# Kernel tuning notes

Hardware: AMD Instinct MI355X
Metric: run time of the kernel (lower is better)

Reference implementation:

```python
import jax, jax.numpy as jnp
import numpy as np

EMBED = 64
HEADS = 4
HEAD_DIM = EMBED // HEADS
N, T = 1024, 36


def setup_inputs() -> dict:
    key = jax.random.key(0)
    ks = jax.random.split(key, 8)
    scale = 1.0 / np.sqrt(HEAD_DIM)
    return {
        "values": jax.random.normal(ks[0], (N, T, EMBED), dtype=jnp.float32),
        "keys": jax.random.normal(ks[1], (N, T, EMBED), dtype=jnp.float32),
        "query": jax.random.normal(ks[2], (N, T, EMBED), dtype=jnp.float32),
        "Wv": jax.random.normal(ks[3], (HEAD_DIM, HEAD_DIM), dtype=jnp.float32) * scale,
        "Wk": jax.random.normal(ks[4], (HEAD_DIM, HEAD_DIM), dtype=jnp.float32) * scale,
        "Wq": jax.random.normal(ks[5], (HEAD_DIM, HEAD_DIM), dtype=jnp.float32) * scale,
        "Wo": jax.random.normal(ks[6], (EMBED, EMBED), dtype=jnp.float32) * (1.0 / np.sqrt(EMBED)),
        "bo": jax.random.normal(ks[7], (EMBED,), dtype=jnp.float32) * 0.01,
    }


def reference(values, keys, query, Wv, Wk, Wq, Wo, bo):
    n, t, c = query.shape
    h, d = HEADS, HEAD_DIM
    v = values.reshape(n, t, h, d)
    k = keys.reshape(n, t, h, d)
    q = query.reshape(n, t, h, d)
    # nn.Linear(head_dim, head_dim, bias=False): x @ W.T
    v = jnp.einsum('nthd,ed->nthe', v, Wv)
    k = jnp.einsum('nthd,ed->nthe', k, Wk)
    q = jnp.einsum('nthd,ed->nthe', q, Wq)
    # attention over the node dim: energy [N_q, N_k, T, H]
    energy = jnp.einsum('qthd,kthd->qkth', q, k)
    attention = jax.nn.softmax(energy / jnp.sqrt(jnp.float32(c)), axis=1)
    out = jnp.einsum('qkth,kthd->qthd', attention, v).reshape(n, t, h * d)
    return out @ Wo.T + bo
```

## Files before the change

kernel.cpp:

```cpp
#include <hip/hip_runtime.h>
#include <math.h>

#define N_NODES 1024
#define T_STEPS 36
#define KTILE   128
#define KSTR2   24
#define VTSTR   136
#define WOS     72
#define OBS2    72
#define YSTR    67

typedef __bf16  bf16x8 __attribute__((ext_vector_type(8)));
typedef float   f32x4  __attribute__((ext_vector_type(4)));

#define MFMA_BF16 __builtin_amdgcn_mfma_f32_16x16x32_bf16
#define PERM_HI 0x07060302u
#define PERM_LO 0x05040100u

__device__ __forceinline__ unsigned short bf16_rne(float f) {
    unsigned int u = __float_as_uint(f);
    u += 0x7FFFu + ((u >> 16) & 1u);
    return (unsigned short)(u >> 16);
}
__device__ __forceinline__ float bf16_tof(unsigned short h) {
    return __uint_as_float(((unsigned int)h) << 16);
}
__device__ __forceinline__ unsigned int split_pack(float a) {
    unsigned short hi = bf16_rne(a);
    unsigned short lo = bf16_rne(a - bf16_tof(hi));
    return ((unsigned int)hi << 16) | lo;
}

__global__ __launch_bounds__(128) void proj5_kernel(
    const float* __restrict__ vin, const float* __restrict__ kin, const float* __restrict__ qin,
    const float* __restrict__ Wv, const float* __restrict__ Wk, const float* __restrict__ Wq,
    unsigned short* __restrict__ qhi, unsigned short* __restrict__ qlo,
    unsigned short* __restrict__ khi, unsigned short* __restrict__ klo,
    unsigned short* __restrict__ vthi, unsigned short* __restrict__ vtlo)
{
    __shared__ float sW[256];
    __shared__ unsigned int ys[128 * YSTR];

    const int tid = threadIdx.x;
    const int mat = blockIdx.y;
    const int nt  = blockIdx.x & 15;
    const int tt  = blockIdx.x >> 4;
    const int n0  = nt * 64, t0 = tt * 2;

    const float* in = (mat == 0) ? vin : (mat == 1) ? kin : qin;
    const float* W  = (mat == 0) ? Wv  : (mat == 1) ? Wk  : Wq;
    sW[tid] = W[tid]; sW[tid + 128] = W[tid + 128];
    __syncthreads();

    {
        const int nl = tid >> 1, tl = tid & 1;
        const size_t p = ((size_t)(n0 + nl)) * T_STEPS + (t0 + tl);
        const float4* src = (const float4*)(in + p * 64);
        float x[64];
        #pragma unroll
        for (int i = 0; i < 16; ++i) {
            float4 f = src[i];
            x[4*i] = f.x; x[4*i+1] = f.y; x[4*i+2] = f.z; x[4*i+3] = f.w;
        }
        const float scale = (mat == 2) ? 0.18033688011112042f : 1.0f;
        unsigned int* yrow = &ys[tid * YSTR];
        #pragma unroll
        for (int e = 0; e < 16; ++e) {
            float4 w0 = *(const float4*)&sW[e*16+0],  w1 = *(const float4*)&sW[e*16+4];
            float4 w2 = *(const float4*)&sW[e*16+8],  w3 = *(const float4*)&sW[e*16+12];
            #pragma unroll
            for (int hd = 0; hd < 4; ++hd) {
                const float* xr = &x[hd*16];
                float a = xr[0]*w0.x;
                a = fmaf(xr[1],w0.y,a);  a = fmaf(xr[2],w0.z,a);  a = fmaf(xr[3],w0.w,a);
                a = fmaf(xr[4],w1.x,a);  a = fmaf(xr[5],w1.y,a);  a = fmaf(xr[6],w1.z,a);  a = fmaf(xr[7],w1.w,a);
                a = fmaf(xr[8],w2.x,a);  a = fmaf(xr[9],w2.y,a);  a = fmaf(xr[10],w2.z,a); a = fmaf(xr[11],w2.w,a);
                a = fmaf(xr[12],w3.x,a); a = fmaf(xr[13],w3.y,a); a = fmaf(xr[14],w3.z,a); a = fmaf(xr[15],w3.w,a);
                yrow[hd*16 + e] = split_pack(a * scale);
            }
        }
    }
    __syncthreads();

    if (mat != 0) {
        unsigned short* ohi = (mat == 1) ? khi : qhi;
        unsigned short* olo = (mat == 1) ? klo : qlo;
        const int nl2 = tid >> 1, eh = tid & 1;
        #pragma unroll
        for (int pass = 0; pass < 8; ++pass) {
            const int tl2 = pass & 1, hd = pass >> 1;
            const unsigned int* yr = &ys[(nl2*2 + tl2) * YSTR + hd*16 + eh*8];
            unsigned int u0 = yr[0], u1 = yr[1], u2 = yr[2], u3 = yr[3];
            unsigned int u4 = yr[4], u5 = yr[5], u6 = yr[6], u7 = yr[7];
            uint4 hi4, lo4;
            hi4.x = __builtin_amdgcn_perm(u1, u0, PERM_HI);
            hi4.y = __builtin_amdgcn_perm(u3, u2, PERM_HI);
            hi4.z = __builtin_amdgcn_perm(u5, u4, PERM_HI);
            hi4.w = __builtin_amdgcn_perm(u7, u6, PERM_HI);
            lo4.x = __builtin_amdgcn_perm(u1, u0, PERM_LO);
            lo4.y = __builtin_amdgcn_perm(u3, u2, PERM_LO);
            lo4.z = __builtin_amdgcn_perm(u5, u4, PERM_LO);
            lo4.w = __builtin_amdgcn_perm(u7, u6, PERM_LO);
            const int th = (t0 + tl2) * 4 + hd;
            const size_t off = ((size_t)th * N_NODES + n0 + nl2) * 16 + eh * 8;
            *(uint4*)(ohi + off) = hi4;
            *(uint4*)(olo + off) = lo4;
        }
    } else {
        const int e = tid >> 3, ng = tid & 7;
        #pragma unroll
        for (int pass = 0; pass < 8; ++pass) {
            const int tl2 = pass & 1, hd = pass >> 1;
            unsigned int u[8];
            #pragma unroll
            for (int j = 0; j < 8; ++j)
                u[j] = ys[((ng*8 + j)*2 + tl2) * YSTR + hd*16 + e];
            uint4 hi4, lo4;
            hi4.x = __builtin_amdgcn_perm(u[1], u[0], PERM_HI);
            hi4.y = __builtin_amdgcn_perm(u[3], u[2], PERM_HI);
            hi4.z = __builtin_amdgcn_perm(u[5], u[4], PERM_HI);
            hi4.w = __builtin_amdgcn_perm(u[7], u[6], PERM_HI);
            lo4.x = __builtin_amdgcn_perm(u[1], u[0], PERM_LO);
            lo4.y = __builtin_amdgcn_perm(u[3], u[2], PERM_LO);
            lo4.z = __builtin_amdgcn_perm(u[5], u[4], PERM_LO);
            lo4.w = __builtin_amdgcn_perm(u[7], u[6], PERM_LO);
            const int th = (t0 + tl2) * 4 + hd;
            const size_t off = ((size_t)th * 16 + e) * N_NODES + n0 + ng * 8;
            *(uint4*)(vthi + off) = hi4;
            *(uint4*)(vtlo + off) = lo4;
        }
    }
}

__global__ __launch_bounds__(128, 4) void attn_mfma4_kernel(
    const unsigned short* __restrict__ qhi, const unsigned short* __restrict__ qlo,
    const unsigned short* __restrict__ khi, const unsigned short* __restrict__ klo,
    const unsigned short* __restrict__ vthi, const unsigned short* __restrict__ vtlo,
    unsigned short* __restrict__ obh, unsigned short* __restrict__ obl)
{
    __shared__ unsigned short khi_s[KTILE * KSTR2];
    __shared__ unsigned short klo_s[KTILE * KSTR2];
    __shared__ unsigned short vthi_s[16 * VTSTR];
    __shared__ unsigned short vtlo_s[16 * VTSTR];

    const int tid  = threadIdx.x;
    const int wave = tid >> 6, lane = tid & 63;
    const int m = lane & 15, quad = lane >> 4;

    const int bid = blockIdx.x;
    const int th  = bid % 144;
    const int qb  = bid / 144;
    const int t   = th >> 2, hd = th & 3;
    const int q0  = qb * 64;
    const size_t base_th = (size_t)th * N_NODES;

    const bf16x8 bzero = {};
    bf16x8 b1q[2], b2q[2];
    #pragma unroll
    for (int g = 0; g < 2; ++g) {
        const int qrow = q0 + wave * 32 + g * 16 + m;
        b1q[g] = *(const bf16x8*)(qhi + (base_th + qrow) * 16 + (quad & 1) * 8);
        b2q[g] = (quad < 2)
            ? *(const bf16x8*)(qlo + (base_th + qrow) * 16 + (quad & 1) * 8) : bzero;
    }

    union { unsigned short su[8]; bf16x8 v; } onesu;
    #pragma unroll
    for (int i = 0; i < 8; ++i) onesu.su[i] = 0x3F80;
    const bf16x8 bones = onesu.v;

    f32x4 og[2]   = {{0.f,0.f,0.f,0.f},{0.f,0.f,0.f,0.f}};
    f32x4 lacc[2] = {{0.f,0.f,0.f,0.f},{0.f,0.f,0.f,0.f}};
    const unsigned short* kbase = (quad < 2) ? khi_s : klo_s;
    const int koff = m * KSTR2 + (quad & 1) * 8;
    const int voff = m * VTSTR + quad * 8;

    const int vsel = tid >> 6, vd = (tid >> 2) & 15, vpart = tid & 3;
    const unsigned short* vsrc0 = (vsel ? vtlo : vthi)
        + ((size_t)th * 16 + vd) * N_NODES + vpart * 32;
    unsigned short* vdst = (vsel ? vtlo_s : vthi_s) + vd * VTSTR + vpart * 32;

    for (int kt = 0; kt < N_NODES; kt += KTILE) {
        __syncthreads();
        {
            const uint4* gh = (const uint4*)(khi + (base_th + kt + tid) * 16);
            const uint4* gl = (const uint4*)(klo + (base_th + kt + tid) * 16);
            uint4 a0 = gh[0], a1 = gh[1], c0 = gl[0], c1 = gl[1];
            *(uint4*)&khi_s[tid * KSTR2]     = a0;
            *(uint4*)&khi_s[tid * KSTR2 + 8] = a1;
            *(uint4*)&klo_s[tid * KSTR2]     = c0;
            *(uint4*)&klo_s[tid * KSTR2 + 8] = c1;
        }
        {
            const unsigned short* src = vsrc0 + kt;
            uint4 a0 = ((const uint4*)src)[0], a1 = ((const uint4*)src)[1];
            uint4 a2 = ((const uint4*)src)[2], a3 = ((const uint4*)src)[3];
            *(uint2*)&vdst[0]  = make_uint2(a0.x, a0.y);
            *(uint2*)&vdst[8]  = make_uint2(a0.z, a0.w);
            *(uint2*)&vdst[16] = make_uint2(a1.x, a1.y);
            *(uint2*)&vdst[24] = make_uint2(a1.z, a1.w);
            *(uint2*)&vdst[4]  = make_uint2(a2.x, a2.y);
            *(uint2*)&vdst[12] = make_uint2(a2.z, a2.w);
            *(uint2*)&vdst[20] = make_uint2(a3.x, a3.y);
            *(uint2*)&vdst[28] = make_uint2(a3.z, a3.w);
        }
        __syncthreads();

        #pragma unroll
        for (int c = 0; c < 4; ++c) {
            bf16x8 a0 = *(const bf16x8*)(kbase + (2*c    ) * 16 * KSTR2 + koff);
            bf16x8 a1 = *(const bf16x8*)(kbase + (2*c + 1) * 16 * KSTR2 + koff);
            bf16x8 vh = *(const bf16x8*)&vthi_s[voff + c * 32];
            bf16x8 vl = *(const bf16x8*)&vtlo_s[voff + c * 32];
            #pragma unroll
            for (int g = 0; g < 2; ++g) {
                f32x4 s0 = MFMA_BF16(a0, b1q[g], (f32x4){0.f,0.f,0.f,0.f}, 0, 0, 0);
                s0 = MFMA_BF16(a0, b2q[g], s0, 0, 0, 0);
                f32x4 s1 = MFMA_BF16(a1, b1q[g], (f32x4){0.f,0.f,0.f,0.f}, 0, 0, 0);
                s1 = MFMA_BF16(a1, b2q[g], s1, 0, 0, 0);
                union { __bf16 b[8]; bf16x8 v; } ap;
                ap.b[0] = (__bf16)__builtin_amdgcn_exp2f(s0[0]);
                ap.b[1] = (__bf16)__builtin_amdgcn_exp2f(s0[1]);
                ap.b[2] = (__bf16)__builtin_amdgcn_exp2f(s0[2]);
                ap.b[3] = (__bf16)__builtin_amdgcn_exp2f(s0[3]);
                ap.b[4] = (__bf16)__builtin_amdgcn_exp2f(s1[0]);
                ap.b[5] = (__bf16)__builtin_amdgcn_exp2f(s1[1]);
                ap.b[6] = (__bf16)__builtin_amdgcn_exp2f(s1[2]);
                ap.b[7] = (__bf16)__builtin_amdgcn_exp2f(s1[3]);
                lacc[g] = MFMA_BF16(ap.v, bones, lacc[g], 0, 0, 0);
                og[g]   = MFMA_BF16(ap.v, vh, og[g], 0, 0, 0);
                og[g]   = MFMA_BF16(ap.v, vl, og[g], 0, 0, 0);
            }
        }
    }

    #pragma unroll
    for (int g = 0; g < 2; ++g) {
        #pragma unroll
        for (int r = 0; r < 4; ++r) {
            const float val = og[g][r] * __builtin_amdgcn_rcpf(lacc[g][r]);
            const int row = q0 + wave * 32 + g * 16 + quad * 4 + r;
            const size_t off = ((size_t)row * T_STEPS + t) * 64 + hd * 16 + m;
            unsigned short hh = bf16_rne(val);
            obh[off] = hh;
            obl[off] = bf16_rne(val - bf16_tof(hh));
        }
    }
}

__global__ __launch_bounds__(256) void outproj_mfma_kernel(
    const unsigned short* __restrict__ obh, const unsigned short* __restrict__ obl,
    const float* __restrict__ Wo, const float* __restrict__ bo,
    float* __restrict__ out)
{
    __shared__ unsigned short woh[64 * WOS], wol[64 * WOS];
    __shared__ unsigned short oth[64 * OBS2], otl[64 * OBS2];
    __shared__ float sb[64];
    const int tid = threadIdx.x;

    #pragma unroll
    for (int i = 0; i < 16; ++i) {
        int idx = tid + 256 * i;
        int r = idx >> 6, c = idx & 63;
        float w = Wo[idx];
        unsigned short hh = bf16_rne(w);
        woh[r * WOS + c] = hh;
        wol[r * WOS + c] = bf16_rne(w - bf16_tof(hh));
    }
    if (tid < 64) sb[tid] = bo[tid];

    const size_t p0 = (size_t)blockIdx.x * 64;
    #pragma unroll
    for (int i = 0; i < 2; ++i) {
        int idx = tid + 256 * i;
        int r = idx >> 3, c = (idx & 7) * 8;
        *(uint4*)&oth[r * OBS2 + c] = *(const uint4*)(obh + (p0 + r) * 64 + c);
        *(uint4*)&otl[r * OBS2 + c] = *(const uint4*)(obl + (p0 + r) * 64 + c);
    }
    __syncthreads();

    const int wave = tid >> 6, lane = tid & 63;
    const int m = lane & 15, quad = lane >> 4;
    const int r0 = wave * 16;

    bf16x8 ah[2], al[2];
    #pragma unroll
    for (int kh = 0; kh < 2; ++kh) {
        ah[kh] = *(const bf16x8*)&oth[(r0 + m) * OBS2 + kh * 32 + quad * 8];
        al[kh] = *(const bf16x8*)&otl[(r0 + m) * OBS2 + kh * 32 + quad * 8];
    }

    f32x4 acc[4] = {{0,0,0,0},{0,0,0,0},{0,0,0,0},{0,0,0,0}};
    #pragma unroll
    for (int jt = 0; jt < 4; ++jt) {
        #pragma unroll
        for (int kh = 0; kh < 2; ++kh) {
            bf16x8 bh = *(const bf16x8*)&woh[(jt * 16 + m) * WOS + kh * 32 + quad * 8];
            bf16x8 bl = *(const bf16x8*)&wol[(jt * 16 + m) * WOS + kh * 32 + quad * 8];
            acc[jt] = MFMA_BF16(ah[kh], bh, acc[jt], 0, 0, 0);
            acc[jt] = MFMA_BF16(al[kh], bh, acc[jt], 0, 0, 0);
            acc[jt] = MFMA_BF16(ah[kh], bl, acc[jt], 0, 0, 0);
        }
    }

    #pragma unroll
    for (int jt = 0; jt < 4; ++jt) {
        const float b = sb[jt * 16 + m];
        #pragma unroll
        for (int r = 0; r < 4; ++r)
            out[(p0 + r0 + quad * 4 + r) * 64 + jt * 16 + m] = acc[jt][r] + b;
    }
}

extern "C" void kernel_launch(void* const* d_in, const int* in_sizes, int n_in,
                              void* d_out, int out_size, void* d_ws, size_t ws_size,
                              hipStream_t stream)
{
    (void)in_sizes; (void)n_in; (void)out_size; (void)ws_size;
    const float* values = (const float*)d_in[0];
    const float* keys   = (const float*)d_in[1];
    const float* query  = (const float*)d_in[2];
    const float* Wv     = (const float*)d_in[3];
    const float* Wk     = (const float*)d_in[4];
    const float* Wq     = (const float*)d_in[5];
    const float* Wo     = (const float*)d_in[6];
    const float* bo     = (const float*)d_in[7];

    const size_t TOT = (size_t)144 * N_NODES * 16;
    unsigned short* ws16 = (unsigned short*)d_ws;
    unsigned short* qhi  = ws16;
    unsigned short* qlo  = ws16 + 1*TOT;
    unsigned short* khi  = ws16 + 2*TOT;
    unsigned short* klo  = ws16 + 3*TOT;
    unsigned short* vthi = ws16 + 4*TOT;
    unsigned short* vtlo = ws16 + 5*TOT;
    unsigned short* obh  = ws16 + 6*TOT;
    unsigned short* obl  = ws16 + 7*TOT;

    proj5_kernel<<<dim3(288, 3), 128, 0, stream>>>(values, keys, query, Wv, Wk, Wq,
                                                   qhi, qlo, khi, klo, vthi, vtlo);
    attn_mfma4_kernel<<<dim3(16 * 144), 128, 0, stream>>>(qhi, qlo, khi, klo, vthi, vtlo,
                                                          obh, obl);
    outproj_mfma_kernel<<<dim3(576), 256, 0, stream>>>(obh, obl, Wo, bo, (float*)d_out);
}
```

Baseline: 138.0 us.

## Read K fragments from global directly, prefetch V tiles, and shrink projection staging

The attention kernel no longer stages K hi/lo tiles through shared memory. Each lane loads its MFMA K fragment straight from global memory, and the V tile for the next iteration is prefetched into registers, which cuts LDS traffic and lets the occupancy hint rise from 4 to 5 blocks. The projection kernel writes Q/K outputs directly from registers and processes V one head at a time through a smaller LDS staging buffer. The trade-off is uncoalesced-ish global fragment loads for K that now rely on cache hits, plus extra barriers in the V projection path.

```diff
diff --git a/kernel.cpp b/kernel.cpp
--- a/kernel.cpp
+++ b/kernel.cpp
@@ -4,11 +4,10 @@
 #define N_NODES 1024
 #define T_STEPS 36
 #define KTILE   128
-#define KSTR2   24
 #define VTSTR   136
 #define WOS     72
 #define OBS2    72
-#define YSTR    67
+#define YSTR6   17
 
 typedef __bf16  bf16x8 __attribute__((ext_vector_type(8)));
 typedef float   f32x4  __attribute__((ext_vector_type(4)));
@@ -25,13 +24,8 @@
 __device__ __forceinline__ float bf16_tof(unsigned short h) {
     return __uint_as_float(((unsigned int)h) << 16);
 }
-__device__ __forceinline__ unsigned int split_pack(float a) {
-    unsigned short hi = bf16_rne(a);
-    unsigned short lo = bf16_rne(a - bf16_tof(hi));
-    return ((unsigned int)hi << 16) | lo;
-}
-
-__global__ __launch_bounds__(128) void proj5_kernel(
+
+__global__ __launch_bounds__(128) void proj6_kernel(
     const float* __restrict__ vin, const float* __restrict__ kin, const float* __restrict__ qin,
     const float* __restrict__ Wv, const float* __restrict__ Wk, const float* __restrict__ Wq,
     unsigned short* __restrict__ qhi, unsigned short* __restrict__ qlo,
@@ -39,7 +33,7 @@
     unsigned short* __restrict__ vthi, unsigned short* __restrict__ vtlo)
 {
     __shared__ float sW[256];
-    __shared__ unsigned int ys[128 * YSTR];
+    __shared__ unsigned int ys[128 * YSTR6];
 
     const int tid = threadIdx.x;
     const int mat = blockIdx.y;
@@ -52,94 +46,103 @@
     sW[tid] = W[tid]; sW[tid + 128] = W[tid + 128];
     __syncthreads();
 
-    {
-        const int nl = tid >> 1, tl = tid & 1;
-        const size_t p = ((size_t)(n0 + nl)) * T_STEPS + (t0 + tl);
-        const float4* src = (const float4*)(in + p * 64);
-        float x[64];
-        #pragma unroll
-        for (int i = 0; i < 16; ++i) {
-            float4 f = src[i];
-            x[4*i] = f.x; x[4*i+1] = f.y; x[4*i+2] = f.z; x[4*i+3] = f.w;
-        }
-        const float scale = (mat == 2) ? 0.18033688011112042f : 1.0f;
-        unsigned int* yrow = &ys[tid * YSTR];
-        #pragma unroll
-        for (int e = 0; e < 16; ++e) {
-            float4 w0 = *(const float4*)&sW[e*16+0],  w1 = *(const float4*)&sW[e*16+4];
-            float4 w2 = *(const float4*)&sW[e*16+8],  w3 = *(const float4*)&sW[e*16+12];
+    const int nl = tid >> 1, tl = tid & 1;
+    const int n = n0 + nl, tcur = t0 + tl;
+    const size_t ib = ((size_t)n * T_STEPS + tcur) * 64;
+    const float scale = (mat == 2) ? 0.18033688011112042f : 1.0f;
+
+    if (mat != 0) {
+        unsigned short* ohi = (mat == 1) ? khi : qhi;
+        unsigned short* olo = (mat == 1) ? klo : qlo;
+        #pragma unroll
+        for (int hd = 0; hd < 4; ++hd) {
+            float xr[16];
             #pragma unroll
-            for (int hd = 0; hd < 4; ++hd) {
-                const float* xr = &x[hd*16];
+            for (int i = 0; i < 4; ++i) {
+                float4 f = *(const float4*)(in + ib + hd*16 + 4*i);
+                xr[4*i] = f.x; xr[4*i+1] = f.y; xr[4*i+2] = f.z; xr[4*i+3] = f.w;
+            }
+            union { unsigned short u[16]; uint4 v[2]; } hb, lb;
+            #pragma unroll
+            for (int e = 0; e < 16; ++e) {
+                float4 w0 = *(const float4*)&sW[e*16+0],  w1 = *(const float4*)&sW[e*16+4];
+                float4 w2 = *(const float4*)&sW[e*16+8],  w3 = *(const float4*)&sW[e*16+12];
                 float a = xr[0]*w0.x;
                 a = fmaf(xr[1],w0.y,a);  a = fmaf(xr[2],w0.z,a);  a = fmaf(xr[3],w0.w,a);
                 a = fmaf(xr[4],w1.x,a);  a = fmaf(xr[5],w1.y,a);  a = fmaf(xr[6],w1.z,a);  a = fmaf(xr[7],w1.w,a);
                 a = fmaf(xr[8],w2.x,a);  a = fmaf(xr[9],w2.y,a);  a = fmaf(xr[10],w2.z,a); a = fmaf(xr[11],w2.w,a);
                 a = fmaf(xr[12],w3.x,a); a = fmaf(xr[13],w3.y,a); a = fmaf(xr[14],w3.z,a); a = fmaf(xr[15],w3.w,a);
-                yrow[hd*16 + e] = split_pack(a * scale);
-            }
-        }
-    }
-    __syncthreads();
-
-    if (mat != 0) {
-        unsigned short* ohi = (mat == 1) ? khi : qhi;
-        unsigned short* olo = (mat == 1) ? klo : qlo;
-        const int nl2 = tid >> 1, eh = tid & 1;
-        #pragma unroll
-        for (int pass = 0; pass < 8; ++pass) {
-            const int tl2 = pass & 1, hd = pass >> 1;
-            const unsigned int* yr = &ys[(nl2*2 + tl2) * YSTR + hd*16 + eh*8];
-            unsigned int u0 = yr[0], u1 = yr[1], u2 = yr[2], u3 = yr[3];
-            unsigned int u4 = yr[4], u5 = yr[5], u6 = yr[6], u7 = yr[7];
-            uint4 hi4, lo4;
-            hi4.x = __builtin_amdgcn_perm(u1, u0, PERM_HI);
-            hi4.y = __builtin_amdgcn_perm(u3, u2, PERM_HI);
-            hi4.z = __builtin_amdgcn_perm(u5, u4, PERM_HI);
-            hi4.w = __builtin_amdgcn_perm(u7, u6, PERM_HI);
-            lo4.x = __builtin_amdgcn_perm(u1, u0, PERM_LO);
-            lo4.y = __builtin_amdgcn_perm(u3, u2, PERM_LO);
-            lo4.z = __builtin_amdgcn_perm(u5, u4, PERM_LO);
-            lo4.w = __builtin_amdgcn_perm(u7, u6, PERM_LO);
-            const int th = (t0 + tl2) * 4 + hd;
-            const size_t off = ((size_t)th * N_NODES + n0 + nl2) * 16 + eh * 8;
-            *(uint4*)(ohi + off) = hi4;
-            *(uint4*)(olo + off) = lo4;
+                a *= scale;
+                unsigned short hh = bf16_rne(a);
+                hb.u[e] = hh; lb.u[e] = bf16_rne(a - bf16_tof(hh));
+            }
+            const int th = tcur * 4 + hd;
+            const size_t off = ((size_t)th * N_NODES + n) * 16;
+            *(uint4*)(ohi + off)     = hb.v[0];
+            *(uint4*)(ohi + off + 8) = hb.v[1];
+            *(uint4*)(olo + off)     = lb.v[0];
+            *(uint4*)(olo + off + 8) = lb.v[1];
         }
     } else {
-        const int e = tid >> 3, ng = tid & 7;
-        #pragma unroll
-        for (int pass = 0; pass < 8; ++pass) {
-            const int tl2 = pass & 1, hd = pass >> 1;
-            unsigned int u[8];
-            #pragma unroll
-            for (int j = 0; j < 8; ++j)
-                u[j] = ys[((ng*8 + j)*2 + tl2) * YSTR + hd*16 + e];
-            uint4 hi4, lo4;
-            hi4.x = __builtin_amdgcn_perm(u[1], u[0], PERM_HI);
-            hi4.y = __builtin_amdgcn_perm(u[3], u[2], PERM_HI);
-            hi4.z = __builtin_amdgcn_perm(u[5], u[4], PERM_HI);
-            hi4.w = __builtin_amdgcn_perm(u[7], u[6], PERM_HI);
-            lo4.x = __builtin_amdgcn_perm(u[1], u[0], PERM_LO);
-            lo4.y = __builtin_amdgcn_perm(u[3], u[2], PERM_LO);
-            lo4.z = __builtin_amdgcn_perm(u[5], u[4], PERM_LO);
-            lo4.w = __builtin_amdgcn_perm(u[7], u[6], PERM_LO);
-            const int th = (t0 + tl2) * 4 + hd;
-            const size_t off = ((size_t)th * 16 + e) * N_NODES + n0 + ng * 8;
-            *(uint4*)(vthi + off) = hi4;
-            *(uint4*)(vtlo + off) = lo4;
-        }
-    }
-}
-
-__global__ __launch_bounds__(128, 4) void attn_mfma4_kernel(
+        #pragma unroll
+        for (int hd = 0; hd < 4; ++hd) {
+            {
+                float xr[16];
+                #pragma unroll
+                for (int i = 0; i < 4; ++i) {
+                    float4 f = *(const float4*)(in + ib + hd*16 + 4*i);
+                    xr[4*i] = f.x; xr[4*i+1] = f.y; xr[4*i+2] = f.z; xr[4*i+3] = f.w;
+                }
+                unsigned int* yrow = &ys[tid * YSTR6];
+                #pragma unroll
+                for (int e = 0; e < 16; ++e) {
+                    float4 w0 = *(const float4*)&sW[e*16+0],  w1 = *(const float4*)&sW[e*16+4];
+                    float4 w2 = *(const float4*)&sW[e*16+8],  w3 = *(const float4*)&sW[e*16+12];
+                    float a = xr[0]*w0.x;
+                    a = fmaf(xr[1],w0.y,a);  a = fmaf(xr[2],w0.z,a);  a = fmaf(xr[3],w0.w,a);
+                    a = fmaf(xr[4],w1.x,a);  a = fmaf(xr[5],w1.y,a);  a = fmaf(xr[6],w1.z,a);  a = fmaf(xr[7],w1.w,a);
+                    a = fmaf(xr[8],w2.x,a);  a = fmaf(xr[9],w2.y,a);  a = fmaf(xr[10],w2.z,a); a = fmaf(xr[11],w2.w,a);
+                    a = fmaf(xr[12],w3.x,a); a = fmaf(xr[13],w3.y,a); a = fmaf(xr[14],w3.z,a); a = fmaf(xr[15],w3.w,a);
+                    unsigned short hh = bf16_rne(a);
+                    unsigned short ll = bf16_rne(a - bf16_tof(hh));
+                    yrow[e] = ((unsigned int)hh << 16) | ll;
+                }
+            }
+            __syncthreads();
+            {
+                const int e = tid >> 3, ng = tid & 7;
+                #pragma unroll
+                for (int tl2 = 0; tl2 < 2; ++tl2) {
+                    unsigned int u[8];
+                    #pragma unroll
+                    for (int j = 0; j < 8; ++j)
+                        u[j] = ys[((ng*8 + j)*2 + tl2) * YSTR6 + e];
+                    uint4 hi4, lo4;
+                    hi4.x = __builtin_amdgcn_perm(u[1], u[0], PERM_HI);
+                    hi4.y = __builtin_amdgcn_perm(u[3], u[2], PERM_HI);
+                    hi4.z = __builtin_amdgcn_perm(u[5], u[4], PERM_HI);
+                    hi4.w = __builtin_amdgcn_perm(u[7], u[6], PERM_HI);
+                    lo4.x = __builtin_amdgcn_perm(u[1], u[0], PERM_LO);
+                    lo4.y = __builtin_amdgcn_perm(u[3], u[2], PERM_LO);
+                    lo4.z = __builtin_amdgcn_perm(u[5], u[4], PERM_LO);
+                    lo4.w = __builtin_amdgcn_perm(u[7], u[6], PERM_LO);
+                    const int th = (t0 + tl2) * 4 + hd;
+                    const size_t off = ((size_t)th * 16 + e) * N_NODES + n0 + ng * 8;
+                    *(uint4*)(vthi + off) = hi4;
+                    *(uint4*)(vtlo + off) = lo4;
+                }
+            }
+            if (hd < 3) __syncthreads();
+        }
+    }
+}
+
+__global__ __launch_bounds__(128, 5) void attn_mfma5_kernel(
     const unsigned short* __restrict__ qhi, const unsigned short* __restrict__ qlo,
     const unsigned short* __restrict__ khi, const unsigned short* __restrict__ klo,
     const unsigned short* __restrict__ vthi, const unsigned short* __restrict__ vtlo,
     unsigned short* __restrict__ obh, unsigned short* __restrict__ obl)
 {
-    __shared__ unsigned short khi_s[KTILE * KSTR2];
-    __shared__ unsigned short klo_s[KTILE * KSTR2];
     __shared__ unsigned short vthi_s[16 * VTSTR];
     __shared__ unsigned short vtlo_s[16 * VTSTR];
 
@@ -171,47 +174,40 @@
 
     f32x4 og[2]   = {{0.f,0.f,0.f,0.f},{0.f,0.f,0.f,0.f}};
     f32x4 lacc[2] = {{0.f,0.f,0.f,0.f},{0.f,0.f,0.f,0.f}};
-    const unsigned short* kbase = (quad < 2) ? khi_s : klo_s;
-    const int koff = m * KSTR2 + (quad & 1) * 8;
-    const int voff = m * VTSTR + quad * 8;
-
-    const int vsel = tid >> 6, vd = (tid >> 2) & 15, vpart = tid & 3;
-    const unsigned short* vsrc0 = (vsel ? vtlo : vthi)
+
+    const unsigned short* kfrag = ((quad < 2) ? khi : klo)
+        + (base_th + m) * 16 + (quad & 1) * 8;
+
+    const int vd = (tid >> 2) & 15, vpart = tid & 3;
+    const unsigned short* vsrc0 = (wave ? vtlo : vthi)
         + ((size_t)th * 16 + vd) * N_NODES + vpart * 32;
-    unsigned short* vdst = (vsel ? vtlo_s : vthi_s) + vd * VTSTR + vpart * 32;
+    unsigned short* vdst = (wave ? vtlo_s : vthi_s) + vd * VTSTR + vpart * 32;
+
+    uint4 pf0, pf1, pf2, pf3;
+    { const uint4* s = (const uint4*)vsrc0; pf0 = s[0]; pf1 = s[1]; pf2 = s[2]; pf3 = s[3]; }
 
     for (int kt = 0; kt < N_NODES; kt += KTILE) {
         __syncthreads();
-        {
-            const uint4* gh = (const uint4*)(khi + (base_th + kt + tid) * 16);
-            const uint4* gl = (const uint4*)(klo + (base_th + kt + tid) * 16);
-            uint4 a0 = gh[0], a1 = gh[1], c0 = gl[0], c1 = gl[1];
-            *(uint4*)&khi_s[tid * KSTR2]     = a0;
-            *(uint4*)&khi_s[tid * KSTR2 + 8] = a1;
-            *(uint4*)&klo_s[tid * KSTR2]     = c0;
-            *(uint4*)&klo_s[tid * KSTR2 + 8] = c1;
-        }
-        {
-            const unsigned short* src = vsrc0 + kt;
-            uint4 a0 = ((const uint4*)src)[0], a1 = ((const uint4*)src)[1];
-            uint4 a2 = ((const uint4*)src)[2], a3 = ((const uint4*)src)[3];
-            *(uint2*)&vdst[0]  = make_uint2(a0.x, a0.y);
-            *(uint2*)&vdst[8]  = make_uint2(a0.z, a0.w);
-            *(uint2*)&vdst[16] = make_uint2(a1.x, a1.y);
-            *(uint2*)&vdst[24] = make_uint2(a1.z, a1.w);
-            *(uint2*)&vdst[4]  = make_uint2(a2.x, a2.y);
-            *(uint2*)&vdst[12] = make_uint2(a2.z, a2.w);
-            *(uint2*)&vdst[20] = make_uint2(a3.x, a3.y);
-            *(uint2*)&vdst[28] = make_uint2(a3.z, a3.w);
-        }
+        *(uint2*)&vdst[0]  = make_uint2(pf0.x, pf0.y);
+        *(uint2*)&vdst[8]  = make_uint2(pf0.z, pf0.w);
+        *(uint2*)&vdst[16] = make_uint2(pf1.x, pf1.y);
+        *(uint2*)&vdst[24] = make_uint2(pf1.z, pf1.w);
+        *(uint2*)&vdst[4]  = make_uint2(pf2.x, pf2.y);
+        *(uint2*)&vdst[12] = make_uint2(pf2.z, pf2.w);
+        *(uint2*)&vdst[20] = make_uint2(pf3.x, pf3.y);
+        *(uint2*)&vdst[28] = make_uint2(pf3.z, pf3.w);
         __syncthreads();
+        if (kt + KTILE < N_NODES) {
+            const uint4* s = (const uint4*)(vsrc0 + kt + KTILE);
+            pf0 = s[0]; pf1 = s[1]; pf2 = s[2]; pf3 = s[3];
+        }
 
         #pragma unroll
         for (int c = 0; c < 4; ++c) {
-            bf16x8 a0 = *(const bf16x8*)(kbase + (2*c    ) * 16 * KSTR2 + koff);
-            bf16x8 a1 = *(const bf16x8*)(kbase + (2*c + 1) * 16 * KSTR2 + koff);
-            bf16x8 vh = *(const bf16x8*)&vthi_s[voff + c * 32];
-            bf16x8 vl = *(const bf16x8*)&vtlo_s[voff + c * 32];
+            bf16x8 a0 = *(const bf16x8*)(kfrag + (size_t)(kt + (2*c    )*16) * 16);
+            bf16x8 a1 = *(const bf16x8*)(kfrag + (size_t)(kt + (2*c + 1)*16) * 16);
+            bf16x8 vh = *(const bf16x8*)&vthi_s[m * VTSTR + quad * 8 + c * 32];
+            bf16x8 vl = *(const bf16x8*)&vtlo_s[m * VTSTR + quad * 8 + c * 32];
             #pragma unroll
             for (int g = 0; g < 2; ++g) {
                 f32x4 s0 = MFMA_BF16(a0, b1q[g], (f32x4){0.f,0.f,0.f,0.f}, 0, 0, 0);
@@ -337,9 +333,9 @@
     unsigned short* obh  = ws16 + 6*TOT;
     unsigned short* obl  = ws16 + 7*TOT;
 
-    proj5_kernel<<<dim3(288, 3), 128, 0, stream>>>(values, keys, query, Wv, Wk, Wq,
+    proj6_kernel<<<dim3(288, 3), 128, 0, stream>>>(values, keys, query, Wv, Wk, Wq,
                                                    qhi, qlo, khi, klo, vthi, vtlo);
-    attn_mfma4_kernel<<<dim3(16 * 144), 128, 0, stream>>>(qhi, qlo, khi, klo, vthi, vtlo,
+    attn_mfma5_kernel<<<dim3(16 * 144), 128, 0, stream>>>(qhi, qlo, khi, klo, vthi, vtlo,
                                                           obh, obl);
     outproj_mfma_kernel<<<dim3(576), 256, 0, stream>>>(obh, obl, Wo, bo, (float*)d_out);
 }
```

Result: no change. 138.7 us (+0.6%).

## Load K fragments directly from global and register-prefetch V tiles

Applied to the files above, without the earlier changes.

The attention kernel no longer stages K hi/lo tiles in shared memory. Each lane now reads its MFMA K fragment straight from global memory. The V tile for the next iteration is prefetched into registers right after the barrier, so its global load overlaps the current tile's MFMA work. The launch-bounds occupancy hint rises from 4 to 5 blocks per CU. This cuts LDS traffic and footprint and hides V load latency, at the cost of K reads that may be less coalesced and more register pressure.

```diff
diff --git a/kernel.cpp b/kernel.cpp
--- a/kernel.cpp
+++ b/kernel.cpp
@@ -4,7 +4,6 @@
 #define N_NODES 1024
 #define T_STEPS 36
 #define KTILE   128
-#define KSTR2   24
 #define VTSTR   136
 #define WOS     72
 #define OBS2    72
@@ -132,14 +131,12 @@
     }
 }
 
-__global__ __launch_bounds__(128, 4) void attn_mfma4_kernel(
+__global__ __launch_bounds__(128, 5) void attn_mfma5_kernel(
     const unsigned short* __restrict__ qhi, const unsigned short* __restrict__ qlo,
     const unsigned short* __restrict__ khi, const unsigned short* __restrict__ klo,
     const unsigned short* __restrict__ vthi, const unsigned short* __restrict__ vtlo,
     unsigned short* __restrict__ obh, unsigned short* __restrict__ obl)
 {
-    __shared__ unsigned short khi_s[KTILE * KSTR2];
-    __shared__ unsigned short klo_s[KTILE * KSTR2];
     __shared__ unsigned short vthi_s[16 * VTSTR];
     __shared__ unsigned short vtlo_s[16 * VTSTR];
 
@@ -171,47 +168,40 @@
 
     f32x4 og[2]   = {{0.f,0.f,0.f,0.f},{0.f,0.f,0.f,0.f}};
     f32x4 lacc[2] = {{0.f,0.f,0.f,0.f},{0.f,0.f,0.f,0.f}};
-    const unsigned short* kbase = (quad < 2) ? khi_s : klo_s;
-    const int koff = m * KSTR2 + (quad & 1) * 8;
-    const int voff = m * VTSTR + quad * 8;
-
-    const int vsel = tid >> 6, vd = (tid >> 2) & 15, vpart = tid & 3;
-    const unsigned short* vsrc0 = (vsel ? vtlo : vthi)
+
+    const unsigned short* kfrag = ((quad < 2) ? khi : klo)
+        + (base_th + m) * 16 + (quad & 1) * 8;
+
+    const int vd = (tid >> 2) & 15, vpart = tid & 3;
+    const unsigned short* vsrc0 = (wave ? vtlo : vthi)
         + ((size_t)th * 16 + vd) * N_NODES + vpart * 32;
-    unsigned short* vdst = (vsel ? vtlo_s : vthi_s) + vd * VTSTR + vpart * 32;
+    unsigned short* vdst = (wave ? vtlo_s : vthi_s) + vd * VTSTR + vpart * 32;
+
+    uint4 pf0, pf1, pf2, pf3;
+    { const uint4* s = (const uint4*)vsrc0; pf0 = s[0]; pf1 = s[1]; pf2 = s[2]; pf3 = s[3]; }
 
     for (int kt = 0; kt < N_NODES; kt += KTILE) {
         __syncthreads();
-        {
-            const uint4* gh = (const uint4*)(khi + (base_th + kt + tid) * 16);
-            const uint4* gl = (const uint4*)(klo + (base_th + kt + tid) * 16);
-            uint4 a0 = gh[0], a1 = gh[1], c0 = gl[0], c1 = gl[1];
-            *(uint4*)&khi_s[tid * KSTR2]     = a0;
-            *(uint4*)&khi_s[tid * KSTR2 + 8] = a1;
-            *(uint4*)&klo_s[tid * KSTR2]     = c0;
-            *(uint4*)&klo_s[tid * KSTR2 + 8] = c1;
-        }
-        {
-            const unsigned short* src = vsrc0 + kt;
-            uint4 a0 = ((const uint4*)src)[0], a1 = ((const uint4*)src)[1];
-            uint4 a2 = ((const uint4*)src)[2], a3 = ((const uint4*)src)[3];
-            *(uint2*)&vdst[0]  = make_uint2(a0.x, a0.y);
-            *(uint2*)&vdst[8]  = make_uint2(a0.z, a0.w);
-            *(uint2*)&vdst[16] = make_uint2(a1.x, a1.y);
-            *(uint2*)&vdst[24] = make_uint2(a1.z, a1.w);
-            *(uint2*)&vdst[4]  = make_uint2(a2.x, a2.y);
-            *(uint2*)&vdst[12] = make_uint2(a2.z, a2.w);
-            *(uint2*)&vdst[20] = make_uint2(a3.x, a3.y);
-            *(uint2*)&vdst[28] = make_uint2(a3.z, a3.w);
-        }
+        *(uint2*)&vdst[0]  = make_uint2(pf0.x, pf0.y);
+        *(uint2*)&vdst[8]  = make_uint2(pf0.z, pf0.w);
+        *(uint2*)&vdst[16] = make_uint2(pf1.x, pf1.y);
+        *(uint2*)&vdst[24] = make_uint2(pf1.z, pf1.w);
+        *(uint2*)&vdst[4]  = make_uint2(pf2.x, pf2.y);
+        *(uint2*)&vdst[12] = make_uint2(pf2.z, pf2.w);
+        *(uint2*)&vdst[20] = make_uint2(pf3.x, pf3.y);
+        *(uint2*)&vdst[28] = make_uint2(pf3.z, pf3.w);
         __syncthreads();
+        if (kt + KTILE < N_NODES) {
+            const uint4* s = (const uint4*)(vsrc0 + kt + KTILE);
+            pf0 = s[0]; pf1 = s[1]; pf2 = s[2]; pf3 = s[3];
+        }
 
         #pragma unroll
         for (int c = 0; c < 4; ++c) {
-            bf16x8 a0 = *(const bf16x8*)(kbase + (2*c    ) * 16 * KSTR2 + koff);
-            bf16x8 a1 = *(const bf16x8*)(kbase + (2*c + 1) * 16 * KSTR2 + koff);
-            bf16x8 vh = *(const bf16x8*)&vthi_s[voff + c * 32];
-            bf16x8 vl = *(const bf16x8*)&vtlo_s[voff + c * 32];
+            bf16x8 a0 = *(const bf16x8*)(kfrag + (size_t)(kt + (2*c    )*16) * 16);
+            bf16x8 a1 = *(const bf16x8*)(kfrag + (size_t)(kt + (2*c + 1)*16) * 16);
+            bf16x8 vh = *(const bf16x8*)&vthi_s[m * VTSTR + quad * 8 + c * 32];
+            bf16x8 vl = *(const bf16x8*)&vtlo_s[m * VTSTR + quad * 8 + c * 32];
             #pragma unroll
             for (int g = 0; g < 2; ++g) {
                 f32x4 s0 = MFMA_BF16(a0, b1q[g], (f32x4){0.f,0.f,0.f,0.f}, 0, 0, 0);
@@ -339,7 +329,7 @@
 
     proj5_kernel<<<dim3(288, 3), 128, 0, stream>>>(values, keys, query, Wv, Wk, Wq,
                                                    qhi, qlo, khi, klo, vthi, vtlo);
-    attn_mfma4_kernel<<<dim3(16 * 144), 128, 0, stream>>>(qhi, qlo, khi, klo, vthi, vtlo,
+    attn_mfma5_kernel<<<dim3(16 * 144), 128, 0, stream>>>(qhi, qlo, khi, klo, vthi, vtlo,
                                                           obh, obl);
     outproj_mfma_kernel<<<dim3(576), 256, 0, stream>>>(obh, obl, Wo, bo, (float*)d_out);
 }
```

Result: faster. 133.5 us (-3.2%).
